# Kernel tuning notes

Hardware: AMD Instinct MI355X
Metric: run time of the kernel (lower is better)

The kernel has to match this reference:

```python
import jax, jax.numpy as jnp
import numpy as np

N_NODES = 500_000
N_EDGES = 8_000_000
N_GRAPHS = 1000


def _mlp(x, w1, b1, w2, b2):
    # Linear -> SELU -> Linear (torch Sequential equivalent)
    return jax.nn.selu(x @ w1 + b1) @ w2 + b2


def setup_inputs() -> dict:
    key = jax.random.key(0)
    ks = jax.random.split(key, 25)
    p = lambda i, shape: jax.random.normal(ks[i], shape, jnp.float32) * 0.1
    return {
        "nodes": jax.random.normal(ks[0], (N_NODES, 1), jnp.float32),
        "edges": jax.random.normal(ks[1], (N_EDGES, 1), jnp.float32),
        "senders": jax.random.randint(ks[2], (N_EDGES,), 0, N_NODES),
        "receivers": jax.random.randint(ks[3], (N_EDGES,), 0, N_NODES),
        "graph_ids": jnp.sort(jax.random.randint(ks[4], (N_NODES,), 0, N_GRAPHS)),
        "num_graphs": N_GRAPHS,
        # permutate_nodes: 2 -> 10 -> 10
        "pn_w1": p(5, (2, 10)), "pn_b1": p(6, (10,)), "pn_w2": p(7, (10, 10)), "pn_b2": p(8, (10,)),
        # update_edges: 11 -> 5 -> 1
        "ue_w1": p(9, (11, 5)), "ue_b1": p(10, (5,)), "ue_w2": p(11, (5, 1)), "ue_b2": p(12, (1,)),
        # permutate_edges: 1 -> 5 -> 10
        "pe_w1": p(13, (1, 5)), "pe_b1": p(14, (5,)), "pe_w2": p(15, (5, 10)), "pe_b2": p(16, (10,)),
        # update_nodes: 11 -> 5 -> 1
        "un_w1": p(17, (11, 5)), "un_b1": p(18, (5,)), "un_w2": p(19, (5, 1)), "un_b2": p(20, (1,)),
        # predict: 11 -> 10 -> 10
        "pr_w1": p(21, (11, 10)), "pr_b1": p(22, (10,)), "pr_w2": p(23, (10, 10)), "pr_b2": p(24, (10,)),
    }


def reference(nodes, edges, pn_w1, pn_b1, pn_w2, pn_b2,
              ue_w1, ue_b1, ue_w2, ue_b2,
              pe_w1, pe_b1, pe_w2, pe_b2,
              un_w1, un_b1, un_w2, un_b2,
              pr_w1, pr_b1, pr_w2, pr_b2,
              senders, receivers, graph_ids, num_graphs):
    # gather node feats to edges: [recv || send] -> (E, 2)
    collected = jnp.concatenate([nodes[receivers], nodes[senders]], axis=-1)
    h1_nodes = _mlp(collected, pn_w1, pn_b1, pn_w2, pn_b2)  # (E, 10)
    h1_edges = edges  # (E, 1)
    for _ in range(3):
        h1_edges = _mlp(jnp.concatenate([h1_edges, h1_nodes], axis=-1),
                        ue_w1, ue_b1, ue_w2, ue_b2)  # (E, 1)
    # edges -> nodes aggregation (sum over receiver)
    edges_of_nodes = jax.ops.segment_sum(h1_edges, receivers, num_segments=nodes.shape[0])  # (N, 1)
    h2_edges = _mlp(edges_of_nodes, pe_w1, pe_b1, pe_w2, pe_b2)  # (N, 10)
    h2_nodes = nodes  # (N, 1)
    for _ in range(3):
        h2_nodes = _mlp(jnp.concatenate([h2_nodes, h2_edges], axis=-1),
                        un_w1, un_b1, un_w2, un_b2)  # (N, 1)
    # nodes -> globals aggregation (sum per graph)
    g = jax.ops.segment_sum(jnp.concatenate([h2_nodes, h2_edges], axis=-1),
                            graph_ids, num_segments=num_graphs)  # (G, 11)
    out = _mlp(g, pr_w1, pr_b1, pr_w2, pr_b2)  # (G, 10)
    return jax.nn.softmax(out, axis=-1)
```

## Files before the change

kernel.cpp:

```cpp
#include <hip/hip_runtime.h>
#include <hip/hip_fp16.h>
#include <math.h>

#define N_NODES_C  500000
#define N_EDGES_C  8000000
#define N_GRAPHS_C 1000
#define NGROUPS_C  (N_EDGES_C / 4)

#define BSHIFT  11
#define BWIDTH  2048
#define NBKT    245

#define EPB     8192
#define GPB     (EPB / 4)
#define NPB     ((N_EDGES_C + EPB - 1) / EPB)
#define SROW    1024

#define GRAPH_ACC_OFF 0
#define FW_OFF        11008
#define STARTS_OFF    11264
#define PAIRS_OFF     (STARTS_OFF + 246 * SROW)
#define WS_WORDS_NEEDED (PAIRS_OFF + NPB * EPB)
#define OLD_NODE_ACC_OFF 11264
#define OLD_ZERO_WORDS   (OLD_NODE_ACC_OFF + N_NODES_C)


__device__ __forceinline__ float selu_f(float x) {
    const float scale = 1.0507009873554805f;
    const float sa    = 1.0507009873554805f * 1.6732632423543772f;
    float neg = sa * (__expf(x) - 1.0f);
    return x > 0.0f ? scale * x : neg;
}

__device__ __forceinline__ void atomAddF(float* p, float v) {
    __hip_atomic_fetch_add(p, v, __ATOMIC_RELAXED, __HIP_MEMORY_SCOPE_AGENT);
}

__device__ __forceinline__ void fuse_weights(
        int t,
        const float* __restrict__ pn_w1, const float* __restrict__ pn_b1,
        const float* __restrict__ pn_w2, const float* __restrict__ pn_b2,
        const float* __restrict__ ue_w1, const float* __restrict__ ue_b1,
        const float* __restrict__ ue_w2, const float* __restrict__ ue_b2,
        const float* __restrict__ pe_w1, const float* __restrict__ pe_b1,
        const float* __restrict__ pe_w2, const float* __restrict__ pe_b2,
        const float* __restrict__ un_w1, const float* __restrict__ un_b1,
        const float* __restrict__ un_w2, const float* __restrict__ un_b2,
        float* __restrict__ fw) {
    if (t < 20) fw[0 + t] = pn_w1[t];
    if (t < 10) fw[20 + t] = pn_b1[t];
    if (t < 50) {
        int j = t / 5, k = t % 5;
        float s = 0.0f;
        for (int m = 0; m < 10; ++m) s += pn_w2[j * 10 + m] * ue_w1[(1 + m) * 5 + k];
        fw[30 + t] = s;
    }
    if (t < 5) {
        float s = ue_b1[t];
        for (int m = 0; m < 10; ++m) s += pn_b2[m] * ue_w1[(1 + m) * 5 + t];
        fw[80 + t] = s;
    }
    if (t < 5)  fw[85 + t]  = ue_w1[t];
    if (t < 5)  fw[90 + t]  = ue_w2[t];
    if (t == 0) fw[95]      = ue_b2[0];
    if (t < 5)  fw[96 + t]  = pe_w1[t];
    if (t < 5)  fw[101 + t] = pe_b1[t];
    if (t < 50) fw[106 + t] = pe_w2[t];
    if (t < 10) fw[156 + t] = pe_b2[t];
    if (t < 25) {
        int j = t / 5, k = t % 5;
        float s = 0.0f;
        for (int m = 0; m < 10; ++m) s += pe_w2[j * 10 + m] * un_w1[(1 + m) * 5 + k];
        fw[166 + t] = s;
    }
    if (t < 5) {
        float s = un_b1[t];
        for (int m = 0; m < 10; ++m) s += pe_b2[m] * un_w1[(1 + m) * 5 + t];
        fw[191 + t] = s;
    }
    if (t < 5)  fw[196 + t] = un_w1[t];
    if (t < 5)  fw[201 + t] = un_w2[t];
    if (t == 0) fw[206]     = un_b2[0];
}

__global__ __launch_bounds__(256) void k_init(
        float* __restrict__ ws,
        const float* pn_w1, const float* pn_b1, const float* pn_w2, const float* pn_b2,
        const float* ue_w1, const float* ue_b1, const float* ue_w2, const float* ue_b2,
        const float* pe_w1, const float* pe_b1, const float* pe_w2, const float* pe_b2,
        const float* un_w1, const float* un_b1, const float* un_w2, const float* un_b2) {
    int i = blockIdx.x * 256 + threadIdx.x;
    if (i < 11000) ws[GRAPH_ACC_OFF + i] = 0.0f;
    if (blockIdx.x == 0)
        fuse_weights(threadIdx.x, pn_w1, pn_b1, pn_w2, pn_b2, ue_w1, ue_b1, ue_w2, ue_b2,
                     pe_w1, pe_b1, pe_w2, pe_b2, un_w1, un_b1, un_w2, un_b2, ws + FW_OFF);
}

__global__ void k_fuse(const float* pn_w1, const float* pn_b1, const float* pn_w2, const float* pn_b2,
                       const float* ue_w1, const float* ue_b1, const float* ue_w2, const float* ue_b2,
                       const float* pe_w1, const float* pe_b1, const float* pe_w2, const float* pe_b2,
                       const float* un_w1, const float* un_b1, const float* un_w2, const float* un_b2,
                       float* fw) {
    fuse_weights(threadIdx.x, pn_w1, pn_b1, pn_w2, pn_b2, ue_w1, ue_b1, ue_w2, ue_b2,
                 pe_w1, pe_b1, pe_w2, pe_b2, un_w1, un_b1, un_w2, un_b2, fw);
}

__global__ void k_final(const float* __restrict__ graph_acc,
                        const float* __restrict__ pr_w1, const float* __restrict__ pr_b1,
                        const float* __restrict__ pr_w2, const float* __restrict__ pr_b2,
                        float* __restrict__ out) {
    int g = blockIdx.x * blockDim.x + threadIdx.x;
    if (g >= N_GRAPHS_C) return;
    float gv[11];
#pragma unroll
    for (int f = 0; f < 11; ++f) gv[f] = graph_acc[g * 11 + f];
    float h[10];
#pragma unroll
    for (int j = 0; j < 10; ++j) {
        float z = pr_b1[j];
#pragma unroll
        for (int f = 0; f < 11; ++f) z = fmaf(gv[f], pr_w1[f * 10 + j], z);
        h[j] = selu_f(z);
    }
    float o[10];
    float mx = -1e30f;
#pragma unroll
    for (int j = 0; j < 10; ++j) {
        float z = pr_b2[j];
#pragma unroll
        for (int m = 0; m < 10; ++m) z = fmaf(h[m], pr_w2[m * 10 + j], z);
        o[j] = z;
        mx = fmaxf(mx, z);
    }
    float sum = 0.0f;
#pragma unroll
    for (int j = 0; j < 10; ++j) { o[j] = __expf(o[j] - mx); sum += o[j]; }
    float inv = 1.0f / sum;
#pragma unroll
    for (int j = 0; j < 10; ++j) out[g * 10 + j] = o[j] * inv;
}


__global__ __launch_bounds__(256) void k_part(
        const float* __restrict__ nodes, const float* __restrict__ edges,
        const int* __restrict__ senders, const int* __restrict__ receivers,
        const float* __restrict__ fw, int* __restrict__ starts_T,
        unsigned int* __restrict__ pairs) {
    __shared__ int hist[256];
    __shared__ int cursorS[256];
    __shared__ uint4 staged4[EPB / 4];
    unsigned int* staged = (unsigned int*)staged4;

    int tid = threadIdx.x;
    int p   = blockIdx.x;
    int gstart = p * GPB;
    int gnum   = NGROUPS_C - gstart;
    if (gnum > GPB) gnum = GPB;

    hist[tid] = 0;
    __syncthreads();

    int4 rv4[8];
#pragma unroll
    for (int r = 0; r < 8; ++r) {
        int idx = r * 256 + tid;
        if (idx < gnum) {
            rv4[r] = ((const int4*)receivers)[gstart + idx];
            atomicAdd(&hist[rv4[r].x >> BSHIFT], 1);
            atomicAdd(&hist[rv4[r].y >> BSHIFT], 1);
            atomicAdd(&hist[rv4[r].z >> BSHIFT], 1);
            atomicAdd(&hist[rv4[r].w >> BSHIFT], 1);
        }
    }
    __syncthreads();

    int orig = hist[tid];
    int val  = orig;
    for (int d = 1; d < 256; d <<= 1) {
        int add = (tid >= d) ? hist[tid - d] : 0;
        __syncthreads();
        if (tid >= d) { val += add; hist[tid] = val; }
        __syncthreads();
    }
    int excl = val - orig;
    cursorS[tid] = excl;
    if (tid < 246) starts_T[tid * SROW + p] = excl;
    __syncthreads();

    float w_pn1[20], b_pn1[10], W_eb[50], b_eb[5], w1r0[5], w2e[5];
#pragma unroll
    for (int j = 0; j < 20; ++j) w_pn1[j] = fw[j];
#pragma unroll
    for (int j = 0; j < 10; ++j) b_pn1[j] = fw[20 + j];
#pragma unroll
    for (int j = 0; j < 50; ++j) W_eb[j] = fw[30 + j];
#pragma unroll
    for (int j = 0; j < 5; ++j) b_eb[j] = fw[80 + j];
#pragma unroll
    for (int j = 0; j < 5; ++j) w1r0[j] = fw[85 + j];
#pragma unroll
    for (int j = 0; j < 5; ++j) w2e[j] = fw[90 + j];
    float b2e = fw[95];

#pragma unroll
    for (int r = 0; r < 8; ++r) {
        int idx = r * 256 + tid;
        if (idx >= gnum) continue;
        int g = gstart + idx;
        float4 e4 = ((const float4*)edges)[g];
        int4  s4 = ((const int4*)senders)[g];
        float ev[4] = {e4.x, e4.y, e4.z, e4.w};
        int   sv[4] = {s4.x, s4.y, s4.z, s4.w};
        int   rv[4] = {rv4[r].x, rv4[r].y, rv4[r].z, rv4[r].w};
        float nsv[4], nrv[4];
#pragma unroll
        for (int u = 0; u < 4; ++u) { nsv[u] = nodes[sv[u]]; nrv[u] = nodes[rv[u]]; }
#pragma unroll
        for (int u = 0; u < 4; ++u) {
            float nr = nrv[u], ns = nsv[u];
            float bs[5];
#pragma unroll
            for (int k = 0; k < 5; ++k) bs[k] = b_eb[k];
#pragma unroll
            for (int j = 0; j < 10; ++j) {
                float z  = fmaf(nr, w_pn1[j], fmaf(ns, w_pn1[10 + j], b_pn1[j]));
                float sz = selu_f(z);
#pragma unroll
                for (int k = 0; k < 5; ++k) bs[k] = fmaf(sz, W_eb[j * 5 + k], bs[k]);
            }
            float e = ev[u];
#pragma unroll
            for (int it = 0; it < 3; ++it) {
                float acc2 = b2e;
#pragma unroll
                for (int k = 0; k < 5; ++k) {
                    float tt = selu_f(fmaf(e, w1r0[k], bs[k]));
                    acc2 = fmaf(tt, w2e[k], acc2);
                }
                e = acc2;
            }
            int bkt  = rv[u] >> BSHIFT;
            int slot = atomicAdd(&cursorS[bkt], 1);
            unsigned int pk = ((unsigned int)(rv[u] & (BWIDTH - 1)) << 16)
                            | (unsigned int)__half_as_ushort(__float2half_rn(e));
            staged[slot] = pk;
        }
    }
    __syncthreads();

    uint4* dst = (uint4*)(pairs + (size_t)p * EPB);
    for (int i = tid; i < gnum; i += 256) dst[i] = staged4[i];
}

__global__ __launch_bounds__(1024) void k_gather(
        const float* __restrict__ nodes, const int* __restrict__ graph_ids,
        const float* __restrict__ fw, const int* __restrict__ starts_T,
        const unsigned int* __restrict__ pairs, float* __restrict__ graph_acc) {
    __shared__ float accf[BWIDTH];
    __shared__ int s0[SROW], s1[SROW];
    __shared__ float garr[16 * 11];
    int tid = threadIdx.x;
    int b   = blockIdx.x;

#pragma unroll
    for (int q = 0; q < BWIDTH / 1024; ++q) accf[q * 1024 + tid] = 0.0f;
    if (tid < 176) garr[tid] = 0.0f;
    for (int i = tid; i < NPB; i += 1024) {
        s0[i] = starts_T[b * SROW + i];
        s1[i] = starts_T[(b + 1) * SROW + i];
    }
    __syncthreads();

    int w = tid >> 6, lane = tid & 63;
    for (int p = w; p < NPB; p += 16) {
        int st = s0[p], en = s1[p];
        const unsigned int* seg = pairs + (size_t)p * EPB + st;
        int cnt = en - st;
        for (int i = lane; i < cnt; i += 64) {
            unsigned int pk = seg[i];
            atomicAdd(&accf[pk >> 16],
                      __half2float(__ushort_as_half((unsigned short)(pk & 0xffff))));
        }
    }
    __syncthreads();

    float w_pe1[5], b_pe1[5], pe_w2[50], pe_b2[10], W_nb[25], b_nb[5], w1r0n[5], w2n[5];
#pragma unroll
    for (int j = 0; j < 5; ++j) w_pe1[j] = fw[96 + j];
#pragma unroll
    for (int j = 0; j < 5; ++j) b_pe1[j] = fw[101 + j];
#pragma unroll
    for (int j = 0; j < 50; ++j) pe_w2[j] = fw[106 + j];
#pragma unroll
    for (int j = 0; j < 10; ++j) pe_b2[j] = fw[156 + j];
#pragma unroll
    for (int j = 0; j < 25; ++j) W_nb[j] = fw[166 + j];
#pragma unroll
    for (int j = 0; j < 5; ++j) b_nb[j] = fw[191 + j];
#pragma unroll
    for (int j = 0; j < 5; ++j) w1r0n[j] = fw[196 + j];
#pragma unroll
    for (int j = 0; j < 5; ++j) w2n[j] = fw[201 + j];
    float b2n = fw[206];

    int gidBase = graph_ids[b << BSHIFT];

#pragma unroll
    for (int q = 0; q < BWIDTH / 1024; ++q) {
        int local = q * 1024 + tid;
        int i = (b << BSHIFT) + local;
        bool valid = i < N_NODES_C;

        float s = accf[local];
        float t5[5];
#pragma unroll
        for (int k = 0; k < 5; ++k) t5[k] = selu_f(fmaf(s, w_pe1[k], b_pe1[k]));
        float he[10];
#pragma unroll
        for (int m = 0; m < 10; ++m) {
            float a = pe_b2[m];
#pragma unroll
            for (int k = 0; k < 5; ++k) a = fmaf(t5[k], pe_w2[k * 10 + m], a);
            he[m] = a;
        }
        float bs[5];
#pragma unroll
        for (int k = 0; k < 5; ++k) {
            float a = b_nb[k];
#pragma unroll
            for (int t = 0; t < 5; ++t) a = fmaf(t5[t], W_nb[t * 5 + k], a);
            bs[k] = a;
        }
        float n = valid ? nodes[i] : 0.0f;
#pragma unroll
        for (int it = 0; it < 3; ++it) {
            float a = b2n;
#pragma unroll
            for (int k = 0; k < 5; ++k) {
                float tt = selu_f(fmaf(n, w1r0n[k], bs[k]));
                a = fmaf(tt, w2n[k], a);
            }
            n = a;
        }

        int gid = valid ? graph_ids[i] : -1;
        if (!valid) {
            n = 0.0f;
#pragma unroll
            for (int m = 0; m < 10; ++m) he[m] = 0.0f;
        }

        int gid0 = __shfl(gid, 0, 64);
        bool allsame = __all(gid == gid0) && (gid0 >= 0);
        if (allsame) {
            float v = n;
#pragma unroll
            for (int off = 32; off > 0; off >>= 1) v += __shfl_down(v, off, 64);
            float vh[10];
#pragma unroll
            for (int m = 0; m < 10; ++m) {
                float ww = he[m];
#pragma unroll
                for (int off = 32; off > 0; off >>= 1) ww += __shfl_down(ww, off, 64);
                vh[m] = ww;
            }
            if ((tid & 63) == 0) {
                int off = gid0 - gidBase;
                if (off >= 0 && off < 16) {
                    atomicAdd(&garr[off * 11 + 0], v);
#pragma unroll
                    for (int m = 0; m < 10; ++m) atomicAdd(&garr[off * 11 + 1 + m], vh[m]);
                } else {
                    atomAddF(&graph_acc[gid0 * 11 + 0], v);
#pragma unroll
                    for (int m = 0; m < 10; ++m) atomAddF(&graph_acc[gid0 * 11 + 1 + m], vh[m]);
                }
            }
        } else if (valid) {
            int off = gid - gidBase;
            if (off >= 0 && off < 16) {
                atomicAdd(&garr[off * 11 + 0], n);
#pragma unroll
                for (int m = 0; m < 10; ++m) atomicAdd(&garr[off * 11 + 1 + m], he[m]);
            } else {
                atomAddF(&graph_acc[gid * 11 + 0], n);
#pragma unroll
                for (int m = 0; m < 10; ++m) atomAddF(&graph_acc[gid * 11 + 1 + m], he[m]);
            }
        }
    }
    __syncthreads();

    if (tid < 176) {
        float v = garr[tid];
        if (v != 0.0f) {
            int off = tid / 11, f = tid - off * 11;
            int gg = gidBase + off;
            if (gg < N_GRAPHS_C) atomAddF(&graph_acc[gg * 11 + f], v);
        }
    }
}


__global__ __launch_bounds__(256) void k_zero(float* __restrict__ ws, int len4) {
    int i = blockIdx.x * 256 + threadIdx.x;
    if (i < len4) ((float4*)ws)[i] = make_float4(0.f, 0.f, 0.f, 0.f);
}

__global__ __launch_bounds__(256) void k_edges(
        const float* __restrict__ nodes, const float* __restrict__ edges,
        const int* __restrict__ senders, const int* __restrict__ receivers,
        const float* __restrict__ fw, float* __restrict__ node_acc) {
    float w_pn1[20], b_pn1[10], W_eb[50], b_eb[5], w1r0[5], w2e[5];
#pragma unroll
    for (int j = 0; j < 20; ++j) w_pn1[j] = fw[j];
#pragma unroll
    for (int j = 0; j < 10; ++j) b_pn1[j] = fw[20 + j];
#pragma unroll
    for (int j = 0; j < 50; ++j) W_eb[j] = fw[30 + j];
#pragma unroll
    for (int j = 0; j < 5; ++j) b_eb[j] = fw[80 + j];
#pragma unroll
    for (int j = 0; j < 5; ++j) w1r0[j] = fw[85 + j];
#pragma unroll
    for (int j = 0; j < 5; ++j) w2e[j] = fw[90 + j];
    float b2e = fw[95];

    int g = blockIdx.x * 256 + threadIdx.x;
    if (g >= N_EDGES_C / 4) return;

    float4 e4 = ((const float4*)edges)[g];
    int4  s4 = ((const int4*)senders)[g];
    int4  r4 = ((const int4*)receivers)[g];
    float ev[4] = {e4.x, e4.y, e4.z, e4.w};
    int   sv[4] = {s4.x, s4.y, s4.z, s4.w};
    int   rv[4] = {r4.x, r4.y, r4.z, r4.w};
    float nsv[4], nrv[4];
#pragma unroll
    for (int u = 0; u < 4; ++u) { nsv[u] = nodes[sv[u]]; nrv[u] = nodes[rv[u]]; }
#pragma unroll
    for (int u = 0; u < 4; ++u) {
        float nr = nrv[u], ns = nsv[u];
        float bs[5];
#pragma unroll
        for (int k = 0; k < 5; ++k) bs[k] = b_eb[k];
#pragma unroll
        for (int j = 0; j < 10; ++j) {
            float z  = fmaf(nr, w_pn1[j], fmaf(ns, w_pn1[10 + j], b_pn1[j]));
            float sz = selu_f(z);
#pragma unroll
            for (int k = 0; k < 5; ++k) bs[k] = fmaf(sz, W_eb[j * 5 + k], bs[k]);
        }
        float e = ev[u];
#pragma unroll
        for (int it = 0; it < 3; ++it) {
            float acc2 = b2e;
#pragma unroll
            for (int k = 0; k < 5; ++k) {
                float tt = selu_f(fmaf(e, w1r0[k], bs[k]));
                acc2 = fmaf(tt, w2e[k], acc2);
            }
            e = acc2;
        }
        atomAddF(&node_acc[rv[u]], e);
    }
}

__global__ __launch_bounds__(256) void k_nodes(
        const float* __restrict__ nodes, const int* __restrict__ graph_ids,
        const float* __restrict__ fw, const float* __restrict__ node_acc,
        float* __restrict__ graph_acc) {
    float w_pe1[5], b_pe1[5], pe_w2[50], pe_b2[10], W_nb[25], b_nb[5], w1r0n[5], w2n[5];
#pragma unroll
    for (int j = 0; j < 5; ++j) w_pe1[j] = fw[96 + j];
#pragma unroll
    for (int j = 0; j < 5; ++j) b_pe1[j] = fw[101 + j];
#pragma unroll
    for (int j = 0; j < 50; ++j) pe_w2[j] = fw[106 + j];
#pragma unroll
    for (int j = 0; j < 10; ++j) pe_b2[j] = fw[156 + j];
#pragma unroll
    for (int j = 0; j < 25; ++j) W_nb[j] = fw[166 + j];
#pragma unroll
    for (int j = 0; j < 5; ++j) b_nb[j] = fw[191 + j];
#pragma unroll
    for (int j = 0; j < 5; ++j) w1r0n[j] = fw[196 + j];
#pragma unroll
    for (int j = 0; j < 5; ++j) w2n[j] = fw[201 + j];
    float b2n = fw[206];

    int i = blockIdx.x * 256 + threadIdx.x;
    bool valid = i < N_NODES_C;
    int ii = valid ? i : (N_NODES_C - 1);

    float s = node_acc[ii];
    float t5[5];
#pragma unroll
    for (int k = 0; k < 5; ++k) t5[k] = selu_f(fmaf(s, w_pe1[k], b_pe1[k]));
    float he[10];
#pragma unroll
    for (int m = 0; m < 10; ++m) {
        float a = pe_b2[m];
#pragma unroll
        for (int k = 0; k < 5; ++k) a = fmaf(t5[k], pe_w2[k * 10 + m], a);
        he[m] = a;
    }
    float bs[5];
#pragma unroll
    for (int k = 0; k < 5; ++k) {
        float a = b_nb[k];
#pragma unroll
        for (int t = 0; t < 5; ++t) a = fmaf(t5[t], W_nb[t * 5 + k], a);
        bs[k] = a;
    }
    float n = nodes[ii];
#pragma unroll
    for (int it = 0; it < 3; ++it) {
        float a = b2n;
#pragma unroll
        for (int k = 0; k < 5; ++k) {
            float tt = selu_f(fmaf(n, w1r0n[k], bs[k]));
            a = fmaf(tt, w2n[k], a);
        }
        n = a;
    }

    int gid = valid ? graph_ids[ii] : -1;
    if (!valid) {
        n = 0.0f;
#pragma unroll
        for (int m = 0; m < 10; ++m) he[m] = 0.0f;
    }

    int gid0 = __shfl(gid, 0, 64);
    bool allsame = __all(gid == gid0) && (gid0 >= 0);
    if (allsame) {
        float v = n;
#pragma unroll
        for (int off = 32; off > 0; off >>= 1) v += __shfl_down(v, off, 64);
        float vh[10];
#pragma unroll
        for (int m = 0; m < 10; ++m) {
            float ww = he[m];
#pragma unroll
            for (int off = 32; off > 0; off >>= 1) ww += __shfl_down(ww, off, 64);
            vh[m] = ww;
        }
        if ((threadIdx.x & 63) == 0) {
            atomAddF(&graph_acc[gid0 * 11 + 0], v);
#pragma unroll
            for (int m = 0; m < 10; ++m) atomAddF(&graph_acc[gid0 * 11 + 1 + m], vh[m]);
        }
    } else if (valid) {
        atomAddF(&graph_acc[gid * 11 + 0], n);
#pragma unroll
        for (int m = 0; m < 10; ++m) atomAddF(&graph_acc[gid * 11 + 1 + m], he[m]);
    }
}


extern "C" void kernel_launch(void* const* d_in, const int* in_sizes, int n_in,
                              void* d_out, int out_size, void* d_ws, size_t ws_size,
                              hipStream_t stream) {
    const float* nodes     = (const float*)d_in[0];
    const float* edges     = (const float*)d_in[1];
    const int*   senders   = (const int*)d_in[2];
    const int*   receivers = (const int*)d_in[3];
    const int*   graph_ids = (const int*)d_in[4];
    const float* pn_w1 = (const float*)d_in[6];
    const float* pn_b1 = (const float*)d_in[7];
    const float* pn_w2 = (const float*)d_in[8];
    const float* pn_b2 = (const float*)d_in[9];
    const float* ue_w1 = (const float*)d_in[10];
    const float* ue_b1 = (const float*)d_in[11];
    const float* ue_w2 = (const float*)d_in[12];
    const float* ue_b2 = (const float*)d_in[13];
    const float* pe_w1 = (const float*)d_in[14];
    const float* pe_b1 = (const float*)d_in[15];
    const float* pe_w2 = (const float*)d_in[16];
    const float* pe_b2 = (const float*)d_in[17];
    const float* un_w1 = (const float*)d_in[18];
    const float* un_b1 = (const float*)d_in[19];
    const float* un_w2 = (const float*)d_in[20];
    const float* un_b2 = (const float*)d_in[21];
    const float* pr_w1 = (const float*)d_in[22];
    const float* pr_b1 = (const float*)d_in[23];
    const float* pr_w2 = (const float*)d_in[24];
    const float* pr_b2 = (const float*)d_in[25];

    float* ws        = (float*)d_ws;
    float* graph_acc = ws + GRAPH_ACC_OFF;
    float* fw        = ws + FW_OFF;
    float* outp      = (float*)d_out;

    if (ws_size >= (size_t)WS_WORDS_NEEDED * 4) {
        int* starts_T        = (int*)ws + STARTS_OFF;
        unsigned int* pairs  = (unsigned int*)ws + PAIRS_OFF;

        hipLaunchKernelGGL(k_init, dim3(44), dim3(256), 0, stream, ws,
                           pn_w1, pn_b1, pn_w2, pn_b2, ue_w1, ue_b1, ue_w2, ue_b2,
                           pe_w1, pe_b1, pe_w2, pe_b2, un_w1, un_b1, un_w2, un_b2);
        hipLaunchKernelGGL(k_part, dim3(NPB), dim3(256), 0, stream,
                           nodes, edges, senders, receivers, fw, starts_T, pairs);
        hipLaunchKernelGGL(k_gather, dim3(NBKT), dim3(1024), 0, stream,
                           nodes, graph_ids, fw, starts_T, pairs, graph_acc);
        hipLaunchKernelGGL(k_final, dim3((N_GRAPHS_C + 255) / 256), dim3(256), 0, stream,
                           graph_acc, pr_w1, pr_b1, pr_w2, pr_b2, outp);
    } else {
        float* node_acc = ws + OLD_NODE_ACC_OFF;
        int len4 = OLD_ZERO_WORDS / 4;
        hipLaunchKernelGGL(k_zero, dim3((len4 + 255) / 256), dim3(256), 0, stream, ws, len4);
        hipLaunchKernelGGL(k_fuse, dim3(1), dim3(64), 0, stream,
                           pn_w1, pn_b1, pn_w2, pn_b2, ue_w1, ue_b1, ue_w2, ue_b2,
                           pe_w1, pe_b1, pe_w2, pe_b2, un_w1, un_b1, un_w2, un_b2, fw);
        hipLaunchKernelGGL(k_edges, dim3((N_EDGES_C / 4 + 255) / 256), dim3(256), 0, stream,
                           nodes, edges, senders, receivers, fw, node_acc);
        hipLaunchKernelGGL(k_nodes, dim3((N_NODES_C + 255) / 256), dim3(256), 0, stream,
                           nodes, graph_ids, fw, node_acc, graph_acc);
        hipLaunchKernelGGL(k_final, dim3((N_GRAPHS_C + 255) / 256), dim3(256), 0, stream,
                           graph_acc, pr_w1, pr_b1, pr_w2, pr_b2, outp);
    }
}
```

Before: 318.1 us.

## Scatter edge pairs into per-bucket global arrays via atomic cursors; use exp2-based SELU

The partition kernel stops writing each block's staged pairs contiguously with a start table. Instead, each block reserves space per bucket in a fixed-capacity global region through atomic cursors and writes its pairs there. The gather kernel can then read one contiguous bucket with vectorised uint4 loads, instead of walking 977 small segments located through a starts table. Separately, the log2(e) factor is folded into the fused weights so SELU can call the hardware exp2 directly. This adds global atomics and silently drops pairs if a bucket overflows the fixed capacity BCAP.

```diff
diff --git a/kernel.cpp b/kernel.cpp
--- a/kernel.cpp
+++ b/kernel.cpp
@@ -10,20 +10,30 @@
 #define BSHIFT  11
 #define BWIDTH  2048
 #define NBKT    245
+#define BCAP    34048
 
 #define EPB     8192
 #define GPB     (EPB / 4)
 #define NPB     ((N_EDGES_C + EPB - 1) / EPB)
-#define SROW    1024
 
 #define GRAPH_ACC_OFF 0
 #define FW_OFF        11008
-#define STARTS_OFF    11264
-#define PAIRS_OFF     (STARTS_OFF + 246 * SROW)
-#define WS_WORDS_NEEDED (PAIRS_OFF + NPB * EPB)
+#define CURSOR_OFF    11264
+#define PAIRS_OFF     11520
+#define WS_WORDS_NEEDED (PAIRS_OFF + NBKT * BCAP)
 #define OLD_NODE_ACC_OFF 11264
 #define OLD_ZERO_WORDS   (OLD_NODE_ACC_OFF + N_NODES_C)
 
+#define LOG2E_F 1.4426950408889634f
+
+
+__device__ __forceinline__ float selu2(float xl) {
+    const float C1 = 0.7282901039f;
+    const float C2 = 1.7580993408473766f;
+    float e = __builtin_amdgcn_exp2f(xl);
+    float neg = fmaf(C2, e, -C2);
+    return xl > 0.0f ? C1 * xl : neg;
+}
 
 __device__ __forceinline__ float selu_f(float x) {
     const float scale = 1.0507009873554805f;
@@ -47,38 +57,39 @@
         const float* __restrict__ un_w1, const float* __restrict__ un_b1,
         const float* __restrict__ un_w2, const float* __restrict__ un_b2,
         float* __restrict__ fw) {
-    if (t < 20) fw[0 + t] = pn_w1[t];
-    if (t < 10) fw[20 + t] = pn_b1[t];
+    const float L = LOG2E_F;
+    if (t < 20) fw[0 + t] = pn_w1[t] * L;
+    if (t < 10) fw[20 + t] = pn_b1[t] * L;
     if (t < 50) {
         int j = t / 5, k = t % 5;
         float s = 0.0f;
         for (int m = 0; m < 10; ++m) s += pn_w2[j * 10 + m] * ue_w1[(1 + m) * 5 + k];
-        fw[30 + t] = s;
+        fw[30 + t] = s * L;
     }
     if (t < 5) {
         float s = ue_b1[t];
         for (int m = 0; m < 10; ++m) s += pn_b2[m] * ue_w1[(1 + m) * 5 + t];
-        fw[80 + t] = s;
-    }
-    if (t < 5)  fw[85 + t]  = ue_w1[t];
+        fw[80 + t] = s * L;
+    }
+    if (t < 5)  fw[85 + t]  = ue_w1[t] * L;
     if (t < 5)  fw[90 + t]  = ue_w2[t];
     if (t == 0) fw[95]      = ue_b2[0];
-    if (t < 5)  fw[96 + t]  = pe_w1[t];
-    if (t < 5)  fw[101 + t] = pe_b1[t];
+    if (t < 5)  fw[96 + t]  = pe_w1[t] * L;
+    if (t < 5)  fw[101 + t] = pe_b1[t] * L;
     if (t < 50) fw[106 + t] = pe_w2[t];
     if (t < 10) fw[156 + t] = pe_b2[t];
     if (t < 25) {
         int j = t / 5, k = t % 5;
         float s = 0.0f;
         for (int m = 0; m < 10; ++m) s += pe_w2[j * 10 + m] * un_w1[(1 + m) * 5 + k];
-        fw[166 + t] = s;
+        fw[166 + t] = s * L;
     }
     if (t < 5) {
         float s = un_b1[t];
         for (int m = 0; m < 10; ++m) s += pe_b2[m] * un_w1[(1 + m) * 5 + t];
-        fw[191 + t] = s;
-    }
-    if (t < 5)  fw[196 + t] = un_w1[t];
+        fw[191 + t] = s * L;
+    }
+    if (t < 5)  fw[196 + t] = un_w1[t] * L;
     if (t < 5)  fw[201 + t] = un_w2[t];
     if (t == 0) fw[206]     = un_b2[0];
 }
@@ -91,6 +102,7 @@
         const float* un_w1, const float* un_b1, const float* un_w2, const float* un_b2) {
     int i = blockIdx.x * 256 + threadIdx.x;
     if (i < 11000) ws[GRAPH_ACC_OFF + i] = 0.0f;
+    if (i < 256) ((int*)ws)[CURSOR_OFF + i] = i * BCAP;
     if (blockIdx.x == 0)
         fuse_weights(threadIdx.x, pn_w1, pn_b1, pn_w2, pn_b2, ue_w1, ue_b1, ue_w2, ue_b2,
                      pe_w1, pe_b1, pe_w2, pe_b2, un_w1, un_b1, un_w2, un_b2, ws + FW_OFF);
@@ -144,12 +156,13 @@
 __global__ __launch_bounds__(256) void k_part(
         const float* __restrict__ nodes, const float* __restrict__ edges,
         const int* __restrict__ senders, const int* __restrict__ receivers,
-        const float* __restrict__ fw, int* __restrict__ starts_T,
+        const float* __restrict__ fw, int* __restrict__ cursor,
         unsigned int* __restrict__ pairs) {
     __shared__ int hist[256];
+    __shared__ int lstart[256];
     __shared__ int cursorS[256];
-    __shared__ uint4 staged4[EPB / 4];
-    unsigned int* staged = (unsigned int*)staged4;
+    __shared__ int gbase[256];
+    __shared__ unsigned int staged[EPB];
 
     int tid = threadIdx.x;
     int p   = blockIdx.x;
@@ -183,8 +196,15 @@
         __syncthreads();
     }
     int excl = val - orig;
+    lstart[tid]  = excl;
     cursorS[tid] = excl;
-    if (tid < 246) starts_T[tid * SROW + p] = excl;
+    if (tid < NBKT) {
+        int gb = (orig > 0)
+            ? __hip_atomic_fetch_add(&cursor[tid], orig, __ATOMIC_RELAXED,
+                                     __HIP_MEMORY_SCOPE_AGENT)
+            : tid * BCAP;
+        gbase[tid] = gb;
+    }
     __syncthreads();
 
     float w_pn1[20], b_pn1[10], W_eb[50], b_eb[5], w1r0[5], w2e[5];
@@ -223,8 +243,8 @@
             for (int k = 0; k < 5; ++k) bs[k] = b_eb[k];
 #pragma unroll
             for (int j = 0; j < 10; ++j) {
-                float z  = fmaf(nr, w_pn1[j], fmaf(ns, w_pn1[10 + j], b_pn1[j]));
-                float sz = selu_f(z);
+                float zl = fmaf(nr, w_pn1[j], fmaf(ns, w_pn1[10 + j], b_pn1[j]));
+                float sz = selu2(zl);
 #pragma unroll
                 for (int k = 0; k < 5; ++k) bs[k] = fmaf(sz, W_eb[j * 5 + k], bs[k]);
             }
@@ -234,7 +254,7 @@
                 float acc2 = b2e;
 #pragma unroll
                 for (int k = 0; k < 5; ++k) {
-                    float tt = selu_f(fmaf(e, w1r0[k], bs[k]));
+                    float tt = selu2(fmaf(e, w1r0[k], bs[k]));
                     acc2 = fmaf(tt, w2e[k], acc2);
                 }
                 e = acc2;
@@ -248,16 +268,24 @@
     }
     __syncthreads();
 
-    uint4* dst = (uint4*)(pairs + (size_t)p * EPB);
-    for (int i = tid; i < gnum; i += 256) dst[i] = staged4[i];
+    int wv = tid >> 6, lane = tid & 63;
+    for (int bkt = wv; bkt < NBKT; bkt += 4) {
+        int st  = lstart[bkt];
+        int cnt = hist[bkt] - st;
+        int gb  = gbase[bkt];
+        int lim = (bkt + 1) * BCAP;
+        for (int i = lane; i < cnt; i += 64) {
+            int d = gb + i;
+            if (d < lim) pairs[d] = staged[st + i];
+        }
+    }
 }
 
 __global__ __launch_bounds__(1024) void k_gather(
         const float* __restrict__ nodes, const int* __restrict__ graph_ids,
-        const float* __restrict__ fw, const int* __restrict__ starts_T,
+        const float* __restrict__ fw, const int* __restrict__ cursor,
         const unsigned int* __restrict__ pairs, float* __restrict__ graph_acc) {
     __shared__ float accf[BWIDTH];
-    __shared__ int s0[SROW], s1[SROW];
     __shared__ float garr[16 * 11];
     int tid = threadIdx.x;
     int b   = blockIdx.x;
@@ -265,22 +293,29 @@
 #pragma unroll
     for (int q = 0; q < BWIDTH / 1024; ++q) accf[q * 1024 + tid] = 0.0f;
     if (tid < 176) garr[tid] = 0.0f;
-    for (int i = tid; i < NPB; i += 1024) {
-        s0[i] = starts_T[b * SROW + i];
-        s1[i] = starts_T[(b + 1) * SROW + i];
-    }
     __syncthreads();
 
-    int w = tid >> 6, lane = tid & 63;
-    for (int p = w; p < NPB; p += 16) {
-        int st = s0[p], en = s1[p];
-        const unsigned int* seg = pairs + (size_t)p * EPB + st;
-        int cnt = en - st;
-        for (int i = lane; i < cnt; i += 64) {
-            unsigned int pk = seg[i];
-            atomicAdd(&accf[pk >> 16],
-                      __half2float(__ushort_as_half((unsigned short)(pk & 0xffff))));
-        }
+    int cnt = cursor[b] - b * BCAP;
+    cnt = cnt < 0 ? 0 : (cnt > BCAP ? BCAP : cnt);
+
+    const unsigned int* base = pairs + (size_t)b * BCAP;
+    const uint4* p4 = (const uint4*)base;
+    int n4 = cnt >> 2;
+    for (int i = tid; i < n4; i += 1024) {
+        uint4 q = p4[i];
+        atomicAdd(&accf[(q.x >> 16) & (BWIDTH - 1)],
+                  __half2float(__ushort_as_half((unsigned short)(q.x & 0xffff))));
+        atomicAdd(&accf[(q.y >> 16) & (BWIDTH - 1)],
+                  __half2float(__ushort_as_half((unsigned short)(q.y & 0xffff))));
+        atomicAdd(&accf[(q.z >> 16) & (BWIDTH - 1)],
+                  __half2float(__ushort_as_half((unsigned short)(q.z & 0xffff))));
+        atomicAdd(&accf[(q.w >> 16) & (BWIDTH - 1)],
+                  __half2float(__ushort_as_half((unsigned short)(q.w & 0xffff))));
+    }
+    if (tid < (cnt & 3)) {
+        unsigned int q = base[(n4 << 2) + tid];
+        atomicAdd(&accf[(q >> 16) & (BWIDTH - 1)],
+                  __half2float(__ushort_as_half((unsigned short)(q & 0xffff))));
     }
     __syncthreads();
 
@@ -314,7 +349,7 @@
         float s = accf[local];
         float t5[5];
 #pragma unroll
-        for (int k = 0; k < 5; ++k) t5[k] = selu_f(fmaf(s, w_pe1[k], b_pe1[k]));
+        for (int k = 0; k < 5; ++k) t5[k] = selu2(fmaf(s, w_pe1[k], b_pe1[k]));
         float he[10];
 #pragma unroll
         for (int m = 0; m < 10; ++m) {
@@ -337,7 +372,7 @@
             float a = b2n;
 #pragma unroll
             for (int k = 0; k < 5; ++k) {
-                float tt = selu_f(fmaf(n, w1r0n[k], bs[k]));
+                float tt = selu2(fmaf(n, w1r0n[k], bs[k]));
                 a = fmaf(tt, w2n[k], a);
             }
             n = a;
@@ -446,8 +481,8 @@
         for (int k = 0; k < 5; ++k) bs[k] = b_eb[k];
 #pragma unroll
         for (int j = 0; j < 10; ++j) {
-            float z  = fmaf(nr, w_pn1[j], fmaf(ns, w_pn1[10 + j], b_pn1[j]));
-            float sz = selu_f(z);
+            float zl = fmaf(nr, w_pn1[j], fmaf(ns, w_pn1[10 + j], b_pn1[j]));
+            float sz = selu2(zl);
 #pragma unroll
             for (int k = 0; k < 5; ++k) bs[k] = fmaf(sz, W_eb[j * 5 + k], bs[k]);
         }
@@ -457,7 +492,7 @@
             float acc2 = b2e;
 #pragma unroll
             for (int k = 0; k < 5; ++k) {
-                float tt = selu_f(fmaf(e, w1r0[k], bs[k]));
+                float tt = selu2(fmaf(e, w1r0[k], bs[k]));
                 acc2 = fmaf(tt, w2e[k], acc2);
             }
             e = acc2;
@@ -496,7 +531,7 @@
     float s = node_acc[ii];
     float t5[5];
 #pragma unroll
-    for (int k = 0; k < 5; ++k) t5[k] = selu_f(fmaf(s, w_pe1[k], b_pe1[k]));
+    for (int k = 0; k < 5; ++k) t5[k] = selu2(fmaf(s, w_pe1[k], b_pe1[k]));
     float he[10];
 #pragma unroll
     for (int m = 0; m < 10; ++m) {
@@ -519,7 +554,7 @@
         float a = b2n;
 #pragma unroll
         for (int k = 0; k < 5; ++k) {
-            float tt = selu_f(fmaf(n, w1r0n[k], bs[k]));
+            float tt = selu2(fmaf(n, w1r0n[k], bs[k]));
             a = fmaf(tt, w2n[k], a);
         }
         n = a;
@@ -594,16 +629,16 @@
     float* outp      = (float*)d_out;
 
     if (ws_size >= (size_t)WS_WORDS_NEEDED * 4) {
-        int* starts_T        = (int*)ws + STARTS_OFF;
+        int* cursor          = (int*)ws + CURSOR_OFF;
         unsigned int* pairs  = (unsigned int*)ws + PAIRS_OFF;
 
         hipLaunchKernelGGL(k_init, dim3(44), dim3(256), 0, stream, ws,
                            pn_w1, pn_b1, pn_w2, pn_b2, ue_w1, ue_b1, ue_w2, ue_b2,
                            pe_w1, pe_b1, pe_w2, pe_b2, un_w1, un_b1, un_w2, un_b2);
         hipLaunchKernelGGL(k_part, dim3(NPB), dim3(256), 0, stream,
-                           nodes, edges, senders, receivers, fw, starts_T, pairs);
+                           nodes, edges, senders, receivers, fw, cursor, pairs);
         hipLaunchKernelGGL(k_gather, dim3(NBKT), dim3(1024), 0, stream,
-                           nodes, graph_ids, fw, starts_T, pairs, graph_acc);
+                           nodes, graph_ids, fw, cursor, pairs, graph_acc);
         hipLaunchKernelGGL(k_final, dim3((N_GRAPHS_C + 255) / 256), dim3(256), 0, stream,
                            graph_acc, pr_w1, pr_b1, pr_w2, pr_b2, outp);
     } else {
```

After: 345.0 us. 1.08x slower.
